# Kernel tuning notes

Hardware: AMD Instinct MI355X
Metric: run time of the kernel (lower is better)

## Reference

```python
import jax, jax.numpy as jnp
import numpy as np

# dims
B, N, M, K = 8, 4096, 1024, 32      # batch, points, centers, neighbors
CIN, CT = 64, 64                    # feature / temb channels
C1, C2 = 64, 128                    # SharedMLP out_channels
G, EPS = 8, 1e-5                    # GroupNorm(8, oc)


def setup_inputs() -> dict:
    key = jax.random.key(0)
    ks = jax.random.split(key, 8)
    return {
        "features": jax.random.normal(ks[0], (B, CIN, N), jnp.float32),
        "coords": jax.random.uniform(ks[1], (B, 3, N), jnp.float32),
        "temb": jax.random.normal(ks[2], (B, CT, N), jnp.float32),
        # SharedMLP params: Conv2d 1x1 -> (O, I) weight, GroupNorm affine
        "W1": jax.random.normal(ks[3], (C1, CIN + 3), jnp.float32) * 0.05,
        "b1": jnp.zeros((C1,), jnp.float32),
        "g1": jnp.ones((C1,), jnp.float32),
        "be1": jnp.zeros((C1,), jnp.float32),
        "W2": jax.random.normal(ks[4], (C2, C1), jnp.float32) * 0.05,
        "b2": jnp.zeros((C2,), jnp.float32),
        "g2": jnp.ones((C2,), jnp.float32),
        "be2": jnp.zeros((C2,), jnp.float32),
    }


def fps_indices(pts):
    # pts: [N, 3] -> [M] indices. Deterministic start at index 0
    # (original uses a random start; math otherwise identical).
    d0 = jnp.sum((pts - pts[0]) ** 2, axis=-1)  # [N]
    def step(dist, _):
        far = jnp.argmax(dist)
        dist = jnp.minimum(dist, jnp.sum((pts - pts[far]) ** 2, axis=-1))
        return dist, far
    _, fars = jax.lax.scan(step, d0, None, length=M - 1)
    return jnp.concatenate([jnp.zeros((1,), fars.dtype), fars])


def group_norm(x, gamma, beta):
    # x: [B, C, M, K], normalize per group over (C//G, M, K)
    b, c, m, k = x.shape
    xr = x.reshape(b, G, c // G, m, k)
    mu = xr.mean(axis=(2, 3, 4), keepdims=True)
    var = xr.var(axis=(2, 3, 4), keepdims=True)
    xn = ((xr - mu) * jax.lax.rsqrt(var + EPS)).reshape(b, c, m, k)
    return xn * gamma[:, None, None] + beta[:, None, None]


def swish(x):
    return x * jax.nn.sigmoid(x)


def reference(features, coords, temb, W1, b1, g1, be1, W2, b2, g2, be2):
    # --- furthest point sampling ---
    idx = jax.vmap(fps_indices)(coords.transpose(0, 2, 1))          # [B, M]
    centers = jax.vmap(lambda c, i: c[:, i])(coords, idx)           # [B, 3, M]
    # --- 'ball query' (actually kNN: source argsorts dist, takes first K) ---
    c = centers.transpose(0, 2, 1)                                  # [B, M, 3]
    p = coords.transpose(0, 2, 1)                                   # [B, N, 3]
    d = (jnp.sum(c * c, -1)[:, :, None] + jnp.sum(p * p, -1)[:, None, :]
         - 2.0 * jnp.einsum('bmd,bnd->bmn', c, p))                  # [B, M, N]
    _, nidx = jax.lax.top_k(-d, K)                                  # [B, M, K]
    gather = jax.vmap(lambda xb, ib: xb[:, ib])                     # [B,C,N],[B,M,K]->[B,C,M,K]
    gcoords = gather(coords, nidx) - centers[..., None]             # [B, 3, M, K]
    gtemb = gather(temb, nidx)                                      # [B, CT, M, K]
    gfeat = jnp.concatenate([gcoords, gather(features, nidx)], axis=1)  # [B, 3+CIN, M, K]
    # --- SharedMLP (1x1 conv -> GN -> Swish) x2, then max over neighbors ---
    h = swish(group_norm(jnp.einsum('oc,bcmk->bomk', W1, gfeat) + b1[:, None, None], g1, be1))
    h = swish(group_norm(jnp.einsum('oc,bcmk->bomk', W2, h) + b2[:, None, None], g2, be2))
    return h.max(axis=-1), centers, gtemb.max(axis=-1)
```

## Files before the change

### kernel.cpp

```cpp
#include <hip/hip_runtime.h>
#include <stdint.h>

#define BB 8
#define NN 4096
#define MM 1024
#define KK 32

__device__ __forceinline__ float bf2f(unsigned short u) {
    union { unsigned int i; float f; } v; v.i = ((unsigned int)u) << 16; return v.f;
}
__device__ __forceinline__ unsigned short f2bf(float f) {
    union { float f; unsigned int i; } v; v.f = f;
    unsigned int x = v.i;
    x += 0x7fffu + ((x >> 16) & 1u);
    return (unsigned short)(x >> 16);
}
__device__ __forceinline__ float swishf(float y) {
    return __fdividef(y, 1.0f + __expf(-y));
}

#define OUT1_OFF 1048576
#define OUT2_OFF 1073152

#define P_W1 0
#define P_B1 4288
#define P_G1 4352
#define P_BE1 4416
#define P_W2 4480
#define P_B2 12672
#define P_G2 12800
#define P_BE2 12928

__device__ __forceinline__ int detect_flag_wave(const unsigned short* f, int lane) {
    unsigned short u = f[lane * 2];
    float x = fabsf(bf2f(u));
    bool ext = (u != 0) && (x > 100.0f || x < 1e-30f);
    unsigned long long m = __ballot(ext);
    return (__popcll(m) >= 16) ? 1 : 0;
}

__global__ __launch_bounds__(256) void k_cvt_all(
    const void* __restrict__ feat, const void* __restrict__ coords,
    float* __restrict__ featT, float* __restrict__ coordsC,
    float* __restrict__ paramsC,
    int* __restrict__ qhead, int* __restrict__ progress,
    const void* W1, const void* b1, const void* g1, const void* be1,
    const void* W2, const void* b2, const void* g2, const void* be2)
{
    __shared__ float tile[64][65];
    __shared__ int sflag;
    int tid = threadIdx.x, blk = blockIdx.x;
    if (tid < 64) {
        int fl0 = detect_flag_wave((const unsigned short*)feat, tid);
        if (tid == 0) sflag = fl0;
    }
    __syncthreads();
    int fl = sflag;
    if (blk == 0) {
        if (tid == 0) *qhead = 0;
        if (tid >= 1 && tid <= 8) progress[(tid - 1) * 16] = -1;
    }
    if (blk < 512) {
        int i = blk;
        int b = i >> 6, n0 = (i & 63) * 64;
        int c = tid >> 2, q = tid & 3;
        size_t base = ((size_t)b * 64 + c) * NN + n0 + q * 16;
        if (fl) {
            const float* sp = (const float*)feat + base;
#pragma unroll
            for (int j = 0; j < 16; j++) tile[c][q * 16 + j] = sp[j];
        } else {
            const unsigned short* sp = (const unsigned short*)feat + base;
#pragma unroll
            for (int j = 0; j < 16; j++) tile[c][q * 16 + j] = bf2f(sp[j]);
        }
        __syncthreads();
        int n = tid >> 2;
        float* dp = featT + ((size_t)b * NN + n0 + n) * 64 + q * 16;
#pragma unroll
        for (int j = 0; j < 16; j++) dp[j] = tile[q * 16 + j][n];
    } else if (blk < 896) {
        int idx = (blk - 512) * 256 + tid;
        coordsC[idx] = fl ? ((const float*)coords)[idx]
                          : bf2f(((const unsigned short*)coords)[idx]);
    } else {
        int idx = (blk - 896) * 256 + tid;
        if (idx < 13056) {
            const void* src; int off;
            if (idx < 4288)       { src = W1;  off = idx; }
            else if (idx < 4352)  { src = b1;  off = idx - 4288; }
            else if (idx < 4416)  { src = g1;  off = idx - 4352; }
            else if (idx < 4480)  { src = be1; off = idx - 4416; }
            else if (idx < 12672) { src = W2;  off = idx - 4480; }
            else if (idx < 12800) { src = b2;  off = idx - 12672; }
            else if (idx < 12928) { src = g2;  off = idx - 12800; }
            else                  { src = be2; off = idx - 12928; }
            paramsC[idx] = fl ? ((const float*)src)[off]
                              : bf2f(((const unsigned short*)src)[off]);
        }
    }
}

struct PW { double d; int p; int q; };
#define PSM_XS   ((float*)(PSM))
#define PSM_YS   ((float*)(PSM + 16384))
#define PSM_ZS   ((float*)(PSM + 32768))
#define PSM_HIST ((int*)(PSM + 49152))
#define PSM_PWB  ((PW*)(PSM + 53248))
#define PSM_SF   ((int*)(PSM + 53376))

#define RESCAN(G) { \
    double gd = 1.0e300; int ga = (G) * 8; \
    _Pragma("unroll") \
    for (int i = 0; i < 8; i++) { \
        int sl = (G) * 8 + i; \
        unsigned int bit = (sl < 32) ? (elo >> sl) : (ehi >> (sl - 32)); \
        double cd = (bit & 1u) ? 1.0e300 : d[sl]; \
        bool rep = cd < gd; \
        gd = rep ? cd : gd; ga = rep ? sl : ga; \
    } \
    g8[(G)] = gd; a8[(G)] = ga; }

__global__ __launch_bounds__(256) void k_fpsknn(
    const void* __restrict__ coords, const float* __restrict__ coordsC,
    float* __restrict__ centersF, int* __restrict__ nidx,
    const void* __restrict__ temb, const void* __restrict__ feat,
    void* __restrict__ d_out,
    int* __restrict__ qhead, int* __restrict__ progress)
{
    __shared__ __align__(16) char PSM[55296];
    int tid = threadIdx.x;
    int blk = blockIdx.x;
    if (tid < 64) {
        int fl0 = detect_flag_wave((const unsigned short*)feat, tid);
        if (tid == 0) *PSM_SF = fl0;
    }
    __syncthreads();
    int fl = *PSM_SF;

    if (blk < 8) {
        int b = blk;
        if (fl) {
            const float* cb = (const float*)coords + (size_t)b * 3 * NN;
#pragma unroll
            for (int i = 0; i < 16; i++) {
                int p = tid + i * 256;
                PSM_XS[p] = cb[p]; PSM_YS[p] = cb[NN + p]; PSM_ZS[p] = cb[2 * NN + p];
            }
        } else {
            const unsigned short* cb = (const unsigned short*)coords + (size_t)b * 3 * NN;
#pragma unroll
            for (int i = 0; i < 16; i++) {
                int p = tid + i * 256;
                PSM_XS[p] = bf2f(cb[p]); PSM_YS[p] = bf2f(cb[NN + p]); PSM_ZS[p] = bf2f(cb[2 * NN + p]);
            }
        }
        if (tid == 0) PSM_HIST[0] = 0;
        __syncthreads();
        if (tid == 0) {
            *(float4*)(centersF + (size_t)b * MM * 4) =
                make_float4(PSM_XS[0], PSM_YS[0], PSM_ZS[0], 0.f);
            __hip_atomic_store(&progress[b * 16], 0, __ATOMIC_RELEASE, __HIP_MEMORY_SCOPE_AGENT);
        }
        int base = tid * 16;
        double px[16], py[16], pz[16], dist[16];
        double x0 = (double)PSM_XS[0], y0 = (double)PSM_YS[0], z0 = (double)PSM_ZS[0];
        double bd = -1.0; int bp = base;
#pragma unroll
        for (int j = 0; j < 16; j++) {
            px[j] = (double)PSM_XS[base + j]; py[j] = (double)PSM_YS[base + j]; pz[j] = (double)PSM_ZS[base + j];
            double dx = px[j] - x0, dy = py[j] - y0, dz = pz[j] - z0;
            dist[j] = fma(dz, dz, fma(dy, dy, dx * dx));
            bool rep = dist[j] > bd;
            bd = rep ? dist[j] : bd; bp = rep ? base + j : bp;
        }
        int lane = tid & 63, wid = tid >> 6;
#pragma unroll 1
        for (int s = 1; s < MM; s++) {
#pragma unroll
            for (int m = 32; m >= 1; m >>= 1) {
                double od = __shfl_xor(bd, m, 64);
                int op = __shfl_xor(bp, m, 64);
                bool rep = (od > bd) || (od == bd && op < bp);
                bd = rep ? od : bd; bp = rep ? op : bp;
            }
            int par = s & 1;
            if (lane == 0) { PW w; w.d = bd; w.p = bp; w.q = 0; PSM_PWB[par * 4 + wid] = w; }
            __syncthreads();
            PW w0 = PSM_PWB[par * 4 + 0];
            double wd = w0.d; int wp = w0.p;
#pragma unroll
            for (int w = 1; w < 4; w++) {
                PW ww = PSM_PWB[par * 4 + w];
                bool rep = (ww.d > wd) || (ww.d == wd && ww.p < wp);
                wd = rep ? ww.d : wd; wp = rep ? ww.p : wp;
            }
            if (tid == 0) PSM_HIST[s] = wp;
            if ((s & 31) == 31 && s >= 63 && wid == ((s >> 5) & 3)) {
                int s0 = s - 63;
                if (lane < 32) {
                    int far = PSM_HIST[s0 + lane];
                    *(float4*)(centersF + ((size_t)b * MM + s0 + lane) * 4) =
                        make_float4(PSM_XS[far], PSM_YS[far], PSM_ZS[far], 0.f);
                }
                if (lane == 0)
                    __hip_atomic_store(&progress[b * 16], s0 + 31,
                                       __ATOMIC_RELEASE, __HIP_MEMORY_SCOPE_AGENT);
            }
            double fx = (double)PSM_XS[wp], fy = (double)PSM_YS[wp], fz = (double)PSM_ZS[wp];
            bd = -1.0; bp = base;
#pragma unroll
            for (int j = 0; j < 16; j++) {
                double dx = px[j] - fx, dy = py[j] - fy, dz = pz[j] - fz;
                double d = fma(dz, dz, fma(dy, dy, dx * dx));
                dist[j] = fmin(dist[j], d);
                bool rep = dist[j] > bd;
                bd = rep ? dist[j] : bd; bp = rep ? base + j : bp;
            }
        }
        __syncthreads();
        if (tid < 32) {
            int far = PSM_HIST[992 + tid];
            *(float4*)(centersF + ((size_t)b * MM + 992 + tid) * 4) =
                make_float4(PSM_XS[far], PSM_YS[far], PSM_ZS[far], 0.f);
        }
        if (tid == 0)
            __hip_atomic_store(&progress[b * 16], 1023,
                               __ATOMIC_RELEASE, __HIP_MEMORY_SCOPE_AGENT);
#pragma unroll
        for (int i = 0; i < 4; i++) {
            int m = tid + i * 256;
            int far = PSM_HIST[m];
            float X = PSM_XS[far], Y = PSM_YS[far], Z = PSM_ZS[far];
            if (fl) {
                float* o = (float*)d_out;
                o[OUT1_OFF + (size_t)(b * 3 + 0) * MM + m] = X;
                o[OUT1_OFF + (size_t)(b * 3 + 1) * MM + m] = Y;
                o[OUT1_OFF + (size_t)(b * 3 + 2) * MM + m] = Z;
            } else {
                unsigned short* o = (unsigned short*)d_out;
                o[OUT1_OFF + (size_t)(b * 3 + 0) * MM + m] = f2bf(X);
                o[OUT1_OFF + (size_t)(b * 3 + 1) * MM + m] = f2bf(Y);
                o[OUT1_OFF + (size_t)(b * 3 + 2) * MM + m] = f2bf(Z);
            }
        }
    } else {
        int lane = tid & 63;
        for (;;) {
            int id = 0;
            if (lane == 0) id = atomicAdd(qhead, 1);
            id = __shfl(id, 0, 64);
            if (id >= BB * MM) break;
            int b = id & 7, m = id >> 3;
            while (__hip_atomic_load(&progress[b * 16], __ATOMIC_ACQUIRE,
                                     __HIP_MEMORY_SCOPE_AGENT) < m)
                __builtin_amdgcn_s_sleep(64);
            int bm = b * MM + m;
            const float* cb = coordsC + (size_t)b * 3 * NN;
            float4 ctr = *(const float4*)(centersF + (size_t)bm * 4);
            double cx = (double)ctr.x, cy = (double)ctr.y, cz = (double)ctr.z;
            double cc = (cx * cx + cy * cy) + cz * cz;
            double d[64];
#pragma unroll 4
            for (int j = 0; j < 64; j++) {
                int p = j * 64 + lane;
                double x = (double)cb[p], y = (double)cb[NN + p], z = (double)cb[2 * NN + p];
                double pp = (x * x + y * y) + z * z;
                double dt = (cx * x + cy * y) + cz * z;
                d[j] = (cc + pp) - 2.0 * dt;
            }
            double g8[8]; int a8[8];
#pragma unroll
            for (int g = 0; g < 8; g++) {
                double gd = d[g * 8]; int ga = g * 8;
#pragma unroll
                for (int i = 1; i < 8; i++) {
                    int sl = g * 8 + i;
                    bool rep = d[sl] < gd;
                    gd = rep ? d[sl] : gd; ga = rep ? sl : ga;
                }
                g8[g] = gd; a8[g] = ga;
            }
            unsigned int elo = 0, ehi = 0;
            int res = 0;
#pragma unroll 1
            for (int it = 0; it < 32; it++) {
                double bd = g8[0]; int ba = a8[0];
#pragma unroll
                for (int g = 1; g < 8; g++) {
                    bool rep = g8[g] < bd;
                    bd = rep ? g8[g] : bd; ba = rep ? a8[g] : ba;
                }
                int bp = ba * 64 + lane;
                double wd = bd; int wp = bp;
#pragma unroll
                for (int s = 32; s >= 1; s >>= 1) {
                    double od = __shfl_xor(wd, s, 64);
                    int op = __shfl_xor(wp, s, 64);
                    bool rep = (od < wd) || (od == wd && op < wp);
                    wd = rep ? od : wd; wp = rep ? op : wp;
                }
                res = (lane == it) ? wp : res;
                if (bp == wp) {
                    int slot = ba;
                    if (slot < 32) elo |= (1u << slot); else ehi |= (1u << (slot - 32));
                    int g = slot >> 3;
                    switch (g) {
                        case 0: RESCAN(0) break;
                        case 1: RESCAN(1) break;
                        case 2: RESCAN(2) break;
                        case 3: RESCAN(3) break;
                        case 4: RESCAN(4) break;
                        case 5: RESCAN(5) break;
                        case 6: RESCAN(6) break;
                        case 7: RESCAN(7) break;
                    }
                }
            }
            if (lane < KK) nidx[(size_t)bm * KK + lane] = res;
            float best = -3.0e38f;
            if (fl) {
                const float* tb = (const float*)temb + ((size_t)b * 64 + lane) * NN;
#pragma unroll 4
                for (int k = 0; k < 32; k++) {
                    int nk = __shfl(res, k, 64);
                    best = fmaxf(best, tb[nk]);
                }
            } else {
                const unsigned short* tb = (const unsigned short*)temb + ((size_t)b * 64 + lane) * NN;
#pragma unroll 4
                for (int k = 0; k < 32; k++) {
                    int nk = __shfl(res, k, 64);
                    best = fmaxf(best, bf2f(tb[nk]));
                }
            }
            size_t off = (size_t)OUT2_OFF + ((size_t)(b * 64 + lane)) * MM + m;
            if (fl) ((float*)d_out)[off] = best;
            else    ((unsigned short*)d_out)[off] = f2bf(best);
        }
    }
}

#define W1Tm(j,c)     (((float*)SM)[(j)*64+(c)])
#define GBUFm(mi,k,c) (((float*)(SM+17152))[(((mi)*32+(k))*66)+(c)])
#define GCm(mi,j,k)   (((float*)(SM+50944))[(((mi)*3+(j))*32)+(k)])
#define NDm(mi,k)     (((int*)(SM+52480))[((mi)*32)+(k)])
#define W2Tm(j,c)     (((float*)SM)[(j)*128+(c)])
#define ACTm(mi,j,k)  (((float*)(SM+32768))[(((mi)*64+(j))*32)+(k)])

__device__ __forceinline__ void mlp1_compute(
    char* SM, int tid, int lane, int mi, int b, int bm,
    const float* __restrict__ featT, const float* __restrict__ coordsC,
    const float* __restrict__ centersF, const int* __restrict__ nidx,
    const float* __restrict__ P, float acc[8][4])
{
    for (int t = tid; t < 64 * 67; t += 256) {
        int c = t / 67, j = t % 67;
        W1Tm(j, c) = P[P_W1 + t];
    }
    if (lane < 32) NDm(mi, lane) = nidx[(size_t)bm * KK + lane] & (NN - 1);
    __syncthreads();
    const float* fb = featT + (size_t)b * NN * 64;
#pragma unroll 4
    for (int q = 0; q < 32; q++) {
        int n = NDm(mi, q);
        GBUFm(mi, q, lane) = fb[(size_t)n * 64 + lane];
    }
    float4 ctr = *(const float4*)(centersF + (size_t)bm * 4);
    const float* cb = coordsC + (size_t)b * 3 * NN;
    if (lane < 32) {
        int n = NDm(mi, lane);
        GCm(mi, 0, lane) = __fsub_rn(cb[n], ctr.x);
        GCm(mi, 1, lane) = __fsub_rn(cb[NN + n], ctr.y);
        GCm(mi, 2, lane) = __fsub_rn(cb[2 * NN + n], ctr.z);
    }
    __syncthreads();
    int c0 = (lane >> 3) * 8;
    int k0 = (lane & 7) * 4;
#pragma unroll
    for (int i = 0; i < 8; i++)
#pragma unroll
        for (int kk = 0; kk < 4; kk++) acc[i][kk] = 0.f;
#pragma unroll
    for (int j = 0; j < 3; j++) {
        float4 a = *(const float4*)&GCm(mi, j, k0);
        float4 w0 = *(const float4*)&W1Tm(j, c0);
        float4 w1v = *(const float4*)&W1Tm(j, c0 + 4);
        float w[8] = {w0.x, w0.y, w0.z, w0.w, w1v.x, w1v.y, w1v.z, w1v.w};
#pragma unroll
        for (int i = 0; i < 8; i++) {
            acc[i][0] = fmaf(w[i], a.x, acc[i][0]);
            acc[i][1] = fmaf(w[i], a.y, acc[i][1]);
            acc[i][2] = fmaf(w[i], a.z, acc[i][2]);
            acc[i][3] = fmaf(w[i], a.w, acc[i][3]);
        }
    }
#pragma unroll 4
    for (int c = 0; c < 64; c++) {
        float f0 = GBUFm(mi, k0 + 0, c);
        float f1 = GBUFm(mi, k0 + 1, c);
        float f2 = GBUFm(mi, k0 + 2, c);
        float f3 = GBUFm(mi, k0 + 3, c);
        int j = 3 + c;
        float4 w0 = *(const float4*)&W1Tm(j, c0);
        float4 w1v = *(const float4*)&W1Tm(j, c0 + 4);
        float w[8] = {w0.x, w0.y, w0.z, w0.w, w1v.x, w1v.y, w1v.z, w1v.w};
#pragma unroll
        for (int i = 0; i < 8; i++) {
            acc[i][0] = fmaf(w[i], f0, acc[i][0]);
            acc[i][1] = fmaf(w[i], f1, acc[i][1]);
            acc[i][2] = fmaf(w[i], f2, acc[i][2]);
            acc[i][3] = fmaf(w[i], f3, acc[i][3]);
        }
    }
}

__device__ __forceinline__ void mlp2_compute(
    char* SM, int tid, int lane, int mi, int b,
    const float acc1[8][4], const float* __restrict__ coef1,
    const float* __restrict__ P, float acc2[16][4])
{
    __syncthreads();
    int c0 = (lane >> 3) * 8;
    int k0 = (lane & 7) * 4;
#pragma unroll
    for (int i = 0; i < 8; i++) {
        int c = c0 + i;
        float sc = coef1[(b * 64 + c) * 2];
        float sh = coef1[(b * 64 + c) * 2 + 1];
        float bb = P[P_B1 + c];
#pragma unroll
        for (int kk = 0; kk < 4; kk++)
            ACTm(mi, c, k0 + kk) = swishf(fmaf(acc1[i][kk] + bb, sc, sh));
    }
    for (int t = tid; t < 128 * 64; t += 256) {
        int c = t >> 6, j = t & 63;
        W2Tm(j, c) = P[P_W2 + t];
    }
    __syncthreads();
    int c02 = (lane >> 3) * 16;
#pragma unroll
    for (int i = 0; i < 16; i++)
#pragma unroll
        for (int kk = 0; kk < 4; kk++) acc2[i][kk] = 0.f;
#pragma unroll 4
    for (int j = 0; j < 64; j++) {
        float4 a = *(const float4*)&ACTm(mi, j, k0);
        float4 w0 = *(const float4*)&W2Tm(j, c02);
        float4 w1v = *(const float4*)&W2Tm(j, c02 + 4);
        float4 w2v = *(const float4*)&W2Tm(j, c02 + 8);
        float4 w3 = *(const float4*)&W2Tm(j, c02 + 12);
        float w[16] = {w0.x, w0.y, w0.z, w0.w, w1v.x, w1v.y, w1v.z, w1v.w,
                       w2v.x, w2v.y, w2v.z, w2v.w, w3.x, w3.y, w3.z, w3.w};
#pragma unroll
        for (int i = 0; i < 16; i++) {
            acc2[i][0] = fmaf(w[i], a.x, acc2[i][0]);
            acc2[i][1] = fmaf(w[i], a.y, acc2[i][1]);
            acc2[i][2] = fmaf(w[i], a.z, acc2[i][2]);
            acc2[i][3] = fmaf(w[i], a.w, acc2[i][3]);
        }
    }
}

__global__ __launch_bounds__(256) void k_mlp1s(
    const float* __restrict__ featT, const float* __restrict__ coordsC,
    const float* __restrict__ centersF, const int* __restrict__ nidx,
    const float* __restrict__ P, float* __restrict__ part1)
{
    __shared__ __align__(16) char smem[53248];
    char* SM = smem;
    int tid = threadIdx.x, blk = blockIdx.x;
    int b = blk >> 8, m0 = (blk & 255) * 4;
    int mi = tid >> 6, lane = tid & 63;
    int bm = b * MM + m0 + mi;
    float acc[8][4];
    mlp1_compute(SM, tid, lane, mi, b, bm, featT, coordsC, centersF, nidx, P, acc);
    int c0 = (lane >> 3) * 8;
    float s = 0.f, s2 = 0.f;
#pragma unroll
    for (int i = 0; i < 8; i++) {
        float bb = P[P_B1 + c0 + i];
#pragma unroll
        for (int kk = 0; kk < 4; kk++) {
            float v = acc[i][kk] + bb;
            s += v; s2 = fmaf(v, v, s2);
        }
    }
    s += __shfl_xor(s, 1, 64); s += __shfl_xor(s, 2, 64); s += __shfl_xor(s, 4, 64);
    s2 += __shfl_xor(s2, 1, 64); s2 += __shfl_xor(s2, 2, 64); s2 += __shfl_xor(s2, 4, 64);
    float* sred = (float*)(SM + 52992);
    __syncthreads();
    if ((lane & 7) == 0) {
        int g = lane >> 3;
        sred[(mi * 8 + g) * 2] = s;
        sred[(mi * 8 + g) * 2 + 1] = s2;
    }
    __syncthreads();
    if (tid < 16) {
        int g = tid >> 1, w = tid & 1;
        float t = sred[(0 * 8 + g) * 2 + w] + sred[(1 * 8 + g) * 2 + w]
                + sred[(2 * 8 + g) * 2 + w] + sred[(3 * 8 + g) * 2 + w];
        part1[blk * 16 + g * 2 + w] = t;
    }
}

__global__ __launch_bounds__(512) void k_coef1(
    const float* __restrict__ part1, const float* __restrict__ P,
    float* __restrict__ coef1)
{
    __shared__ float red[512];
    int tid = threadIdx.x;
    int out = tid >> 2, sub = tid & 3;
    int b = out >> 4, gw = out & 15;
    const float* p = part1 + (size_t)(b * 256 + sub * 64) * 16 + gw;
    float s = 0.f;
#pragma unroll 8
    for (int r = 0; r < 64; r++) s += p[r * 16];
    red[out * 4 + sub] = s;
    __syncthreads();
    if (tid < 64) {
        int bb = tid >> 3, g = tid & 7;
        int o1 = (bb * 16 + g * 2) * 4, o2 = o1 + 4;
        float S = red[o1] + red[o1 + 1] + red[o1 + 2] + red[o1 + 3];
        float Q = red[o2] + red[o2 + 1] + red[o2 + 2] + red[o2 + 3];
        float inv_n = 1.0f / 262144.0f;
        float mean = S * inv_n;
        float var = Q * inv_n - mean * mean;
        float inv = rsqrtf(var + 1e-5f);
        for (int i = 0; i < 8; i++) {
            int c = g * 8 + i;
            float sc = P[P_G1 + c] * inv;
            coef1[(bb * 64 + c) * 2] = sc;
            coef1[(bb * 64 + c) * 2 + 1] = P[P_BE1 + c] - mean * sc;
        }
    }
}

__global__ __launch_bounds__(256) void k_mlp2s(
    const float* __restrict__ featT, const float* __restrict__ coordsC,
    const float* __restrict__ centersF, const int* __restrict__ nidx,
    const float* __restrict__ P, const float* __restrict__ coef1,
    float* __restrict__ part2)
{
    __shared__ __align__(16) char smem[65536];
    char* SM = smem;
    int tid = threadIdx.x, blk = blockIdx.x;
    int b = blk >> 8, m0 = (blk & 255) * 4;
    int mi = tid >> 6, lane = tid & 63;
    int bm = b * MM + m0 + mi;
    float acc1[8][4];
    mlp1_compute(SM, tid, lane, mi, b, bm, featT, coordsC, centersF, nidx, P, acc1);
    float acc2[16][4];
    mlp2_compute(SM, tid, lane, mi, b, acc1, coef1, P, acc2);
    int c02 = (lane >> 3) * 16;
    float s = 0.f, s2 = 0.f;
#pragma unroll
    for (int i = 0; i < 16; i++) {
        float bb = P[P_B2 + c02 + i];
#pragma unroll
        for (int kk = 0; kk < 4; kk++) {
            float v = acc2[i][kk] + bb;
            s += v; s2 = fmaf(v, v, s2);
        }
    }
    s += __shfl_xor(s, 1, 64); s += __shfl_xor(s, 2, 64); s += __shfl_xor(s, 4, 64);
    s2 += __shfl_xor(s2, 1, 64); s2 += __shfl_xor(s2, 2, 64); s2 += __shfl_xor(s2, 4, 64);
    __syncthreads();
    float* sred = (float*)SM;
    if ((lane & 7) == 0) {
        int g = lane >> 3;
        sred[(mi * 8 + g) * 2] = s;
        sred[(mi * 8 + g) * 2 + 1] = s2;
    }
    __syncthreads();
    if (tid < 16) {
        int g = tid >> 1, w = tid & 1;
        float t = sred[(0 * 8 + g) * 2 + w] + sred[(1 * 8 + g) * 2 + w]
                + sred[(2 * 8 + g) * 2 + w] + sred[(3 * 8 + g) * 2 + w];
        part2[blk * 16 + g * 2 + w] = t;
    }
}

__global__ __launch_bounds__(512) void k_coef2(
    const float* __restrict__ part2, const float* __restrict__ P,
    float* __restrict__ coef2)
{
    __shared__ float red[512];
    int tid = threadIdx.x;
    int out = tid >> 2, sub = tid & 3;
    int b = out >> 4, gw = out & 15;
    const float* p = part2 + (size_t)(b * 256 + sub * 64) * 16 + gw;
    float s = 0.f;
#pragma unroll 8
    for (int r = 0; r < 64; r++) s += p[r * 16];
    red[out * 4 + sub] = s;
    __syncthreads();
    if (tid < 64) {
        int bb = tid >> 3, g = tid & 7;
        int o1 = (bb * 16 + g * 2) * 4, o2 = o1 + 4;
        float S = red[o1] + red[o1 + 1] + red[o1 + 2] + red[o1 + 3];
        float Q = red[o2] + red[o2 + 1] + red[o2 + 2] + red[o2 + 3];
        float inv_n = 1.0f / 524288.0f;
        float mean = S * inv_n;
        float var = Q * inv_n - mean * mean;
        float inv = rsqrtf(var + 1e-5f);
        for (int i = 0; i < 16; i++) {
            int c = g * 16 + i;
            float sc = P[P_G2 + c] * inv;
            coef2[(bb * 128 + c) * 2] = sc;
            coef2[(bb * 128 + c) * 2 + 1] = P[P_BE2 + c] - mean * sc;
        }
    }
}

__global__ __launch_bounds__(256) void k_final(
    const float* __restrict__ featT, const float* __restrict__ coordsC,
    const float* __restrict__ centersF, const int* __restrict__ nidx,
    const float* __restrict__ P, const float* __restrict__ coef1,
    const float* __restrict__ coef2,
    void* __restrict__ d_out, const void* __restrict__ feat)
{
    __shared__ __align__(16) char smem[65536];
    char* SM = smem;
    int tid = threadIdx.x, blk = blockIdx.x;
    if (tid < 64) {
        int fl0 = detect_flag_wave((const unsigned short*)feat, tid);
        if (tid == 0) *(int*)(SM + 53248) = fl0;
    }
    __syncthreads();
    int fl = *(int*)(SM + 53248);
    int b = blk >> 8, m0 = (blk & 255) * 4;
    int mi = tid >> 6, lane = tid & 63;
    int bm = b * MM + m0 + mi;
    float acc1[8][4];
    mlp1_compute(SM, tid, lane, mi, b, bm, featT, coordsC, centersF, nidx, P, acc1);
    float acc2[16][4];
    mlp2_compute(SM, tid, lane, mi, b, acc1, coef1, P, acc2);
    int c02 = (lane >> 3) * 16;
    float mx[16];
#pragma unroll
    for (int i = 0; i < 16; i++) {
        int c = c02 + i;
        float sc = coef2[(b * 128 + c) * 2];
        float sh = coef2[(b * 128 + c) * 2 + 1];
        float bb = P[P_B2 + c];
        float v = -3.0e38f;
#pragma unroll
        for (int kk = 0; kk < 4; kk++)
            v = fmaxf(v, swishf(fmaf(acc2[i][kk] + bb, sc, sh)));
        v = fmaxf(v, __shfl_xor(v, 1, 64));
        v = fmaxf(v, __shfl_xor(v, 2, 64));
        v = fmaxf(v, __shfl_xor(v, 4, 64));
        mx[i] = v;
    }
    if ((lane & 7) == 0) {
        int m = m0 + mi;
#pragma unroll
        for (int i = 0; i < 16; i++) {
            size_t off = (size_t)(b * 128 + c02 + i) * MM + m;
            if (fl) ((float*)d_out)[off] = mx[i];
            else    ((unsigned short*)d_out)[off] = f2bf(mx[i]);
        }
    }
}

extern "C" void kernel_launch(void* const* d_in, const int* in_sizes, int n_in,
                              void* d_out, int out_size, void* d_ws, size_t ws_size,
                              hipStream_t stream) {
    (void)in_sizes; (void)n_in; (void)out_size; (void)ws_size;
    const void* feat = d_in[0];
    const void* coords = d_in[1];
    const void* temb = d_in[2];

    char* ws = (char*)d_ws;
    int* qhead = (int*)ws;
    int* progress = (int*)(ws + 512);
    float* coordsC = (float*)(ws + 1088);
    float* paramsC = (float*)(ws + 394304);
    float* centersF = (float*)(ws + 446528);
    int* nidx = (int*)(ws + 577600);
    float* part1 = (float*)(ws + 1626176);
    float* part2 = (float*)(ws + 1757248);
    float* coef1 = (float*)(ws + 1888320);
    float* coef2 = (float*)(ws + 1892416);
    float* featT = (float*)(ws + 1900608);

    k_cvt_all<<<947, 256, 0, stream>>>(feat, coords, featT, coordsC, paramsC,
                                       qhead, progress,
                                       d_in[3], d_in[4], d_in[5], d_in[6],
                                       d_in[7], d_in[8], d_in[9], d_in[10]);
    k_fpsknn<<<256, 256, 0, stream>>>(coords, coordsC, centersF, nidx, temb,
                                      feat, d_out, qhead, progress);
    k_mlp1s<<<2048, 256, 0, stream>>>(featT, coordsC, centersF, nidx, paramsC, part1);
    k_coef1<<<1, 512, 0, stream>>>(part1, paramsC, coef1);
    k_mlp2s<<<2048, 256, 0, stream>>>(featT, coordsC, centersF, nidx, paramsC, coef1, part2);
    k_coef2<<<1, 512, 0, stream>>>(part2, paramsC, coef2);
    k_final<<<2048, 256, 0, stream>>>(featT, coordsC, centersF, nidx, paramsC, coef1, coef2, d_out, feat);
}
```

Before: 1.650 ms.

## Fuse MLP1 GroupNorm statistics into kNN workers and drop coef kernels

The per-center first conv layer and its GroupNorm sum and sum-of-squares move into the kNN worker loop of the FPS/kNN kernel, accumulated into global stats with atomics. This removes the separate k_mlp1s pass and both single-block coef reduction kernels. The downstream kernels now derive scale and shift directly from the raw stats. The cost is extra per-item work inside the persistent kNN workers, float atomics whose summation order is nondeterministic, and the spin-wait reads progress with a relaxed load followed by an acquire load.

```diff
diff --git a/kernel.cpp b/kernel.cpp
--- a/kernel.cpp
+++ b/kernel.cpp
@@ -44,6 +44,7 @@
     float* __restrict__ featT, float* __restrict__ coordsC,
     float* __restrict__ paramsC,
     int* __restrict__ qhead, int* __restrict__ progress,
+    float* __restrict__ stats1,
     const void* W1, const void* b1, const void* g1, const void* be1,
     const void* W2, const void* b2, const void* g2, const void* be2)
 {
@@ -58,7 +59,9 @@
     int fl = sflag;
     if (blk == 0) {
         if (tid == 0) *qhead = 0;
-        if (tid >= 1 && tid <= 8) progress[(tid - 1) * 16] = -1;
+        if (tid < 8) progress[tid * 16] = -1;
+        stats1[tid] = 0.f;
+        stats1[tid + 256] = 0.f;
     }
     if (blk < 512) {
         int i = blk;
@@ -101,13 +104,20 @@
     }
 }
 
+#define W1Tm(j,c)     (((float*)SM)[(j)*64+(c)])
+#define GBUFm(mi,k,c) (((float*)(SM+17152))[(((mi)*32+(k))*66)+(c)])
+#define GCm(mi,j,k)   (((float*)(SM+50944))[(((mi)*3+(j))*32)+(k)])
+#define NDm(mi,k)     (((int*)(SM+52480))[((mi)*32)+(k)])
+#define W2Tm(j,c)     (((float*)SM)[(j)*128+(c)])
+#define ACTm(mi,j,k)  (((float*)(SM+32768))[(((mi)*64+(j))*32)+(k)])
+
 struct PW { double d; int p; int q; };
-#define PSM_XS   ((float*)(PSM))
-#define PSM_YS   ((float*)(PSM + 16384))
-#define PSM_ZS   ((float*)(PSM + 32768))
-#define PSM_HIST ((int*)(PSM + 49152))
-#define PSM_PWB  ((PW*)(PSM + 53248))
-#define PSM_SF   ((int*)(PSM + 53376))
+#define PSM_XS   ((float*)(SM))
+#define PSM_YS   ((float*)(SM + 16384))
+#define PSM_ZS   ((float*)(SM + 32768))
+#define PSM_HIST ((int*)(SM + 49152))
+#define PSM_PWB  ((PW*)(SM + 53248))
+#define PSM_SF   ((int*)(SM + 53376))
 
 #define RESCAN(G) { \
     double gd = 1.0e300; int ga = (G) * 8; \
@@ -125,10 +135,12 @@
     const void* __restrict__ coords, const float* __restrict__ coordsC,
     float* __restrict__ centersF, int* __restrict__ nidx,
     const void* __restrict__ temb, const void* __restrict__ feat,
+    const float* __restrict__ featT, const float* __restrict__ paramsC,
+    float* __restrict__ stats1,
     void* __restrict__ d_out,
     int* __restrict__ qhead, int* __restrict__ progress)
 {
-    __shared__ __align__(16) char PSM[55296];
+    __shared__ __align__(16) char SM[55296];
     int tid = threadIdx.x;
     int blk = blockIdx.x;
     if (tid < 64) {
@@ -245,16 +257,23 @@
             }
         }
     } else {
-        int lane = tid & 63;
+        int lane = tid & 63, wid = tid >> 6;
+        for (int t = tid; t < 64 * 67; t += 256) {
+            int c = t / 67, j = t % 67;
+            W1Tm(j, c) = paramsC[P_W1 + t];
+        }
+        __syncthreads();
         for (;;) {
             int id = 0;
             if (lane == 0) id = atomicAdd(qhead, 1);
             id = __shfl(id, 0, 64);
             if (id >= BB * MM) break;
             int b = id & 7, m = id >> 3;
-            while (__hip_atomic_load(&progress[b * 16], __ATOMIC_ACQUIRE,
+            while (__hip_atomic_load(&progress[b * 16], __ATOMIC_RELAXED,
                                      __HIP_MEMORY_SCOPE_AGENT) < m)
                 __builtin_amdgcn_s_sleep(64);
+            (void)__hip_atomic_load(&progress[b * 16], __ATOMIC_ACQUIRE,
+                                    __HIP_MEMORY_SCOPE_AGENT);
             int bm = b * MM + m;
             const float* cb = coordsC + (size_t)b * 3 * NN;
             float4 ctr = *(const float4*)(centersF + (size_t)bm * 4);
@@ -337,16 +356,78 @@
             size_t off = (size_t)OUT2_OFF + ((size_t)(b * 64 + lane)) * MM + m;
             if (fl) ((float*)d_out)[off] = best;
             else    ((unsigned short*)d_out)[off] = f2bf(best);
-        }
-    }
-}
-
-#define W1Tm(j,c)     (((float*)SM)[(j)*64+(c)])
-#define GBUFm(mi,k,c) (((float*)(SM+17152))[(((mi)*32+(k))*66)+(c)])
-#define GCm(mi,j,k)   (((float*)(SM+50944))[(((mi)*3+(j))*32)+(k)])
-#define NDm(mi,k)     (((int*)(SM+52480))[((mi)*32)+(k)])
-#define W2Tm(j,c)     (((float*)SM)[(j)*128+(c)])
-#define ACTm(mi,j,k)  (((float*)(SM+32768))[(((mi)*64+(j))*32)+(k)])
+            if (lane < 32) NDm(wid, lane) = res & (NN - 1);
+            const float* fb = featT + (size_t)b * NN * 64;
+#pragma unroll 4
+            for (int q = 0; q < 32; q++) {
+                int n = NDm(wid, q);
+                GBUFm(wid, q, lane) = fb[(size_t)n * 64 + lane];
+            }
+            if (lane < 32) {
+                int n = NDm(wid, lane);
+                GCm(wid, 0, lane) = __fsub_rn(cb[n], ctr.x);
+                GCm(wid, 1, lane) = __fsub_rn(cb[NN + n], ctr.y);
+                GCm(wid, 2, lane) = __fsub_rn(cb[2 * NN + n], ctr.z);
+            }
+            int c0 = (lane >> 3) * 8;
+            int k0 = (lane & 7) * 4;
+            float acc[8][4];
+#pragma unroll
+            for (int i = 0; i < 8; i++)
+#pragma unroll
+                for (int kk = 0; kk < 4; kk++) acc[i][kk] = 0.f;
+#pragma unroll
+            for (int j = 0; j < 3; j++) {
+                float4 a = *(const float4*)&GCm(wid, j, k0);
+                float4 w0 = *(const float4*)&W1Tm(j, c0);
+                float4 w1v = *(const float4*)&W1Tm(j, c0 + 4);
+                float w[8] = {w0.x, w0.y, w0.z, w0.w, w1v.x, w1v.y, w1v.z, w1v.w};
+#pragma unroll
+                for (int i = 0; i < 8; i++) {
+                    acc[i][0] = fmaf(w[i], a.x, acc[i][0]);
+                    acc[i][1] = fmaf(w[i], a.y, acc[i][1]);
+                    acc[i][2] = fmaf(w[i], a.z, acc[i][2]);
+                    acc[i][3] = fmaf(w[i], a.w, acc[i][3]);
+                }
+            }
+#pragma unroll 4
+            for (int c = 0; c < 64; c++) {
+                float f0 = GBUFm(wid, k0 + 0, c);
+                float f1 = GBUFm(wid, k0 + 1, c);
+                float f2 = GBUFm(wid, k0 + 2, c);
+                float f3 = GBUFm(wid, k0 + 3, c);
+                int j = 3 + c;
+                float4 w0 = *(const float4*)&W1Tm(j, c0);
+                float4 w1v = *(const float4*)&W1Tm(j, c0 + 4);
+                float w[8] = {w0.x, w0.y, w0.z, w0.w, w1v.x, w1v.y, w1v.z, w1v.w};
+#pragma unroll
+                for (int i = 0; i < 8; i++) {
+                    acc[i][0] = fmaf(w[i], f0, acc[i][0]);
+                    acc[i][1] = fmaf(w[i], f1, acc[i][1]);
+                    acc[i][2] = fmaf(w[i], f2, acc[i][2]);
+                    acc[i][3] = fmaf(w[i], f3, acc[i][3]);
+                }
+            }
+            float s = 0.f, s2 = 0.f;
+#pragma unroll
+            for (int i = 0; i < 8; i++) {
+                float bb = paramsC[P_B1 + c0 + i];
+#pragma unroll
+                for (int kk = 0; kk < 4; kk++) {
+                    float v = acc[i][kk] + bb;
+                    s += v; s2 = fmaf(v, v, s2);
+                }
+            }
+            s += __shfl_xor(s, 1, 64); s += __shfl_xor(s, 2, 64); s += __shfl_xor(s, 4, 64);
+            s2 += __shfl_xor(s2, 1, 64); s2 += __shfl_xor(s2, 2, 64); s2 += __shfl_xor(s2, 4, 64);
+            if ((lane & 7) == 0) {
+                int g = lane >> 3;
+                atomicAdd(&stats1[(b * 8 + g) * 2], s);
+                atomicAdd(&stats1[(b * 8 + g) * 2 + 1], s2);
+            }
+        }
+    }
+}
 
 __device__ __forceinline__ void mlp1_compute(
     char* SM, int tid, int lane, int mi, int b, int bm,
@@ -417,17 +498,22 @@
 
 __device__ __forceinline__ void mlp2_compute(
     char* SM, int tid, int lane, int mi, int b,
-    const float acc1[8][4], const float* __restrict__ coef1,
+    const float acc1[8][4], const float* __restrict__ S1,
     const float* __restrict__ P, float acc2[16][4])
 {
     __syncthreads();
     int c0 = (lane >> 3) * 8;
     int k0 = (lane & 7) * 4;
+    int g = c0 >> 3;
+    float S = S1[(b * 8 + g) * 2], Q = S1[(b * 8 + g) * 2 + 1];
+    float mean = S * (1.0f / 262144.0f);
+    float var = Q * (1.0f / 262144.0f) - mean * mean;
+    float inv = rsqrtf(var + 1e-5f);
 #pragma unroll
     for (int i = 0; i < 8; i++) {
         int c = c0 + i;
-        float sc = coef1[(b * 64 + c) * 2];
-        float sh = coef1[(b * 64 + c) * 2 + 1];
+        float sc = P[P_G1 + c] * inv;
+        float sh = P[P_BE1 + c] - mean * sc;
         float bb = P[P_B1 + c];
 #pragma unroll
         for (int kk = 0; kk < 4; kk++)
@@ -462,85 +548,11 @@
     }
 }
 
-__global__ __launch_bounds__(256) void k_mlp1s(
-    const float* __restrict__ featT, const float* __restrict__ coordsC,
-    const float* __restrict__ centersF, const int* __restrict__ nidx,
-    const float* __restrict__ P, float* __restrict__ part1)
-{
-    __shared__ __align__(16) char smem[53248];
-    char* SM = smem;
-    int tid = threadIdx.x, blk = blockIdx.x;
-    int b = blk >> 8, m0 = (blk & 255) * 4;
-    int mi = tid >> 6, lane = tid & 63;
-    int bm = b * MM + m0 + mi;
-    float acc[8][4];
-    mlp1_compute(SM, tid, lane, mi, b, bm, featT, coordsC, centersF, nidx, P, acc);
-    int c0 = (lane >> 3) * 8;
-    float s = 0.f, s2 = 0.f;
-#pragma unroll
-    for (int i = 0; i < 8; i++) {
-        float bb = P[P_B1 + c0 + i];
-#pragma unroll
-        for (int kk = 0; kk < 4; kk++) {
-            float v = acc[i][kk] + bb;
-            s += v; s2 = fmaf(v, v, s2);
-        }
-    }
-    s += __shfl_xor(s, 1, 64); s += __shfl_xor(s, 2, 64); s += __shfl_xor(s, 4, 64);
-    s2 += __shfl_xor(s2, 1, 64); s2 += __shfl_xor(s2, 2, 64); s2 += __shfl_xor(s2, 4, 64);
-    float* sred = (float*)(SM + 52992);
-    __syncthreads();
-    if ((lane & 7) == 0) {
-        int g = lane >> 3;
-        sred[(mi * 8 + g) * 2] = s;
-        sred[(mi * 8 + g) * 2 + 1] = s2;
-    }
-    __syncthreads();
-    if (tid < 16) {
-        int g = tid >> 1, w = tid & 1;
-        float t = sred[(0 * 8 + g) * 2 + w] + sred[(1 * 8 + g) * 2 + w]
-                + sred[(2 * 8 + g) * 2 + w] + sred[(3 * 8 + g) * 2 + w];
-        part1[blk * 16 + g * 2 + w] = t;
-    }
-}
-
-__global__ __launch_bounds__(512) void k_coef1(
-    const float* __restrict__ part1, const float* __restrict__ P,
-    float* __restrict__ coef1)
-{
-    __shared__ float red[512];
-    int tid = threadIdx.x;
-    int out = tid >> 2, sub = tid & 3;
-    int b = out >> 4, gw = out & 15;
-    const float* p = part1 + (size_t)(b * 256 + sub * 64) * 16 + gw;
-    float s = 0.f;
-#pragma unroll 8
-    for (int r = 0; r < 64; r++) s += p[r * 16];
-    red[out * 4 + sub] = s;
-    __syncthreads();
-    if (tid < 64) {
-        int bb = tid >> 3, g = tid & 7;
-        int o1 = (bb * 16 + g * 2) * 4, o2 = o1 + 4;
-        float S = red[o1] + red[o1 + 1] + red[o1 + 2] + red[o1 + 3];
-        float Q = red[o2] + red[o2 + 1] + red[o2 + 2] + red[o2 + 3];
-        float inv_n = 1.0f / 262144.0f;
-        float mean = S * inv_n;
-        float var = Q * inv_n - mean * mean;
-        float inv = rsqrtf(var + 1e-5f);
-        for (int i = 0; i < 8; i++) {
-            int c = g * 8 + i;
-            float sc = P[P_G1 + c] * inv;
-            coef1[(bb * 64 + c) * 2] = sc;
-            coef1[(bb * 64 + c) * 2 + 1] = P[P_BE1 + c] - mean * sc;
-        }
-    }
-}
-
 __global__ __launch_bounds__(256) void k_mlp2s(
     const float* __restrict__ featT, const float* __restrict__ coordsC,
     const float* __restrict__ centersF, const int* __restrict__ nidx,
-    const float* __restrict__ P, const float* __restrict__ coef1,
-    float* __restrict__ part2)
+    const float* __restrict__ P, const float* __restrict__ stats1,
+    float* __restrict__ stats2)
 {
     __shared__ __align__(16) char smem[65536];
     char* SM = smem;
@@ -551,7 +563,7 @@
     float acc1[8][4];
     mlp1_compute(SM, tid, lane, mi, b, bm, featT, coordsC, centersF, nidx, P, acc1);
     float acc2[16][4];
-    mlp2_compute(SM, tid, lane, mi, b, acc1, coef1, P, acc2);
+    mlp2_compute(SM, tid, lane, mi, b, acc1, stats1, P, acc2);
     int c02 = (lane >> 3) * 16;
     float s = 0.f, s2 = 0.f;
 #pragma unroll
@@ -577,47 +589,15 @@
         int g = tid >> 1, w = tid & 1;
         float t = sred[(0 * 8 + g) * 2 + w] + sred[(1 * 8 + g) * 2 + w]
                 + sred[(2 * 8 + g) * 2 + w] + sred[(3 * 8 + g) * 2 + w];
-        part2[blk * 16 + g * 2 + w] = t;
-    }
-}
-
-__global__ __launch_bounds__(512) void k_coef2(
-    const float* __restrict__ part2, const float* __restrict__ P,
-    float* __restrict__ coef2)
-{
-    __shared__ float red[512];
-    int tid = threadIdx.x;
-    int out = tid >> 2, sub = tid & 3;
-    int b = out >> 4, gw = out & 15;
-    const float* p = part2 + (size_t)(b * 256 + sub * 64) * 16 + gw;
-    float s = 0.f;
-#pragma unroll 8
-    for (int r = 0; r < 64; r++) s += p[r * 16];
-    red[out * 4 + sub] = s;
-    __syncthreads();
-    if (tid < 64) {
-        int bb = tid >> 3, g = tid & 7;
-        int o1 = (bb * 16 + g * 2) * 4, o2 = o1 + 4;
-        float S = red[o1] + red[o1 + 1] + red[o1 + 2] + red[o1 + 3];
-        float Q = red[o2] + red[o2 + 1] + red[o2 + 2] + red[o2 + 3];
-        float inv_n = 1.0f / 524288.0f;
-        float mean = S * inv_n;
-        float var = Q * inv_n - mean * mean;
-        float inv = rsqrtf(var + 1e-5f);
-        for (int i = 0; i < 16; i++) {
-            int c = g * 16 + i;
-            float sc = P[P_G2 + c] * inv;
-            coef2[(bb * 128 + c) * 2] = sc;
-            coef2[(bb * 128 + c) * 2 + 1] = P[P_BE2 + c] - mean * sc;
-        }
+        atomicAdd(&stats2[(b * 8 + g) * 2 + w], t);
     }
 }
 
 __global__ __launch_bounds__(256) void k_final(
     const float* __restrict__ featT, const float* __restrict__ coordsC,
     const float* __restrict__ centersF, const int* __restrict__ nidx,
-    const float* __restrict__ P, const float* __restrict__ coef1,
-    const float* __restrict__ coef2,
+    const float* __restrict__ P, const float* __restrict__ stats1,
+    const float* __restrict__ stats2,
     void* __restrict__ d_out, const void* __restrict__ feat)
 {
     __shared__ __align__(16) char smem[65536];
@@ -635,14 +615,19 @@
     float acc1[8][4];
     mlp1_compute(SM, tid, lane, mi, b, bm, featT, coordsC, centersF, nidx, P, acc1);
     float acc2[16][4];
-    mlp2_compute(SM, tid, lane, mi, b, acc1, coef1, P, acc2);
+    mlp2_compute(SM, tid, lane, mi, b, acc1, stats1, P, acc2);
     int c02 = (lane >> 3) * 16;
+    int g2 = c02 >> 4;
+    float S = stats2[(b * 8 + g2) * 2], Q = stats2[(b * 8 + g2) * 2 + 1];
+    float mean = S * (1.0f / 524288.0f);
+    float var = Q * (1.0f / 524288.0f) - mean * mean;
+    float inv = rsqrtf(var + 1e-5f);
     float mx[16];
 #pragma unroll
     for (int i = 0; i < 16; i++) {
         int c = c02 + i;
-        float sc = coef2[(b * 128 + c) * 2];
-        float sh = coef2[(b * 128 + c) * 2 + 1];
+        float sc = P[P_G2 + c] * inv;
+        float sh = P[P_BE2 + c] - mean * sc;
         float bb = P[P_B2 + c];
         float v = -3.0e38f;
 #pragma unroll
@@ -675,25 +660,23 @@
     char* ws = (char*)d_ws;
     int* qhead = (int*)ws;
     int* progress = (int*)(ws + 512);
-    float* coordsC = (float*)(ws + 1088);
-    float* paramsC = (float*)(ws + 394304);
-    float* centersF = (float*)(ws + 446528);
-    int* nidx = (int*)(ws + 577600);
-    float* part1 = (float*)(ws + 1626176);
-    float* part2 = (float*)(ws + 1757248);
-    float* coef1 = (float*)(ws + 1888320);
-    float* coef2 = (float*)(ws + 1892416);
-    float* featT = (float*)(ws + 1900608);
+    float* stats1 = (float*)(ws + 1024);
+    float* stats2 = (float*)(ws + 2048);
+    float* coordsC = (float*)(ws + 3072);
+    float* paramsC = (float*)(ws + 396288);
+    float* centersF = (float*)(ws + 448512);
+    int* nidx = (int*)(ws + 579584);
+    float* featT = (float*)(ws + 1628160);
 
     k_cvt_all<<<947, 256, 0, stream>>>(feat, coords, featT, coordsC, paramsC,
-                                       qhead, progress,
+                                       qhead, progress, stats1,
                                        d_in[3], d_in[4], d_in[5], d_in[6],
                                        d_in[7], d_in[8], d_in[9], d_in[10]);
     k_fpsknn<<<256, 256, 0, stream>>>(coords, coordsC, centersF, nidx, temb,
-                                      feat, d_out, qhead, progress);
-    k_mlp1s<<<2048, 256, 0, stream>>>(featT, coordsC, centersF, nidx, paramsC, part1);
-    k_coef1<<<1, 512, 0, stream>>>(part1, paramsC, coef1);
-    k_mlp2s<<<2048, 256, 0, stream>>>(featT, coordsC, centersF, nidx, paramsC, coef1, part2);
-    k_coef2<<<1, 512, 0, stream>>>(part2, paramsC, coef2);
-    k_final<<<2048, 256, 0, stream>>>(featT, coordsC, centersF, nidx, paramsC, coef1, coef2, d_out, feat);
-}
+                                      feat, featT, paramsC, stats1, d_out,
+                                      qhead, progress);
+    k_mlp2s<<<2048, 256, 0, stream>>>(featT, coordsC, centersF, nidx, paramsC,
+                                      stats1, stats2);
+    k_final<<<2048, 256, 0, stream>>>(featT, coordsC, centersF, nidx, paramsC,
+                                      stats1, stats2, d_out, feat);
+}
```

After: 1.540 ms. 6.7% less time.
